# Kernel optimization log

Measured on AMD Instinct MI355X. Metric: run time of the kernel, lower is better.

The kernel has to match this reference:

```python
import jax, jax.numpy as jnp
import numpy as np

NUM_HEADS = 16
HIDDEN = 1024
HEAD = HIDDEN // NUM_HEADS


def setup_inputs() -> dict:
    key = jax.random.key(0)
    k1, k2, k3, k4, k5 = jax.random.split(key, 5)
    b, s, d = 2, 2048, HIDDEN
    scale = 1.0 / np.sqrt(d)
    return {
        "features": jax.random.normal(k1, (b, s, d), dtype=jnp.float32),
        "qkv_w": jax.random.normal(k2, (3 * d, d), dtype=jnp.float32) * scale,  # torch Linear weight [out,in]
        "qkv_b": jax.random.normal(k3, (3 * d,), dtype=jnp.float32) * 0.01,
        "out_w": jax.random.normal(k4, (d, d), dtype=jnp.float32) * scale,
        "out_b": jax.random.normal(k5, (d,), dtype=jnp.float32) * 0.01,
        "use_causal_mask": 0,
    }


def reference(features, qkv_w, qkv_b, out_w, out_b, use_causal_mask):
    b, s, d = features.shape
    qkv = features @ qkv_w.T + qkv_b                      # [b,s,3d]
    q, k, v = jnp.split(qkv, 3, axis=-1)
    # [b,s,d] -> [b,h,s,hd]
    def heads(x):
        return x.reshape(b, s, NUM_HEADS, HEAD).transpose(0, 2, 1, 3)
    q, k, v = heads(q), heads(k), heads(v)
    scores = jnp.einsum("bhqd,bhkd->bhqk", q, k) / np.sqrt(HEAD)
    if use_causal_mask:
        mask = jnp.triu(jnp.ones((s, s), dtype=bool), k=1)
        scores = jnp.where(mask, -jnp.inf, scores)
    attn = jax.nn.softmax(scores, axis=-1)
    out = jnp.einsum("bhqk,bhkd->bhqd", attn, v)          # [b,h,s,hd]
    out = out.transpose(0, 2, 1, 3).reshape(b, s, d)
    return out @ out_w.T + out_b
```

## Files before the change

### kernel.cpp

```cpp
#include <hip/hip_runtime.h>
#include <math.h>

#define BATCH 2
#define SEQ   2048
#define HID   1024
#define NHEAD 16
#define ROWS  (BATCH*SEQ)
#define QKV_N (3*HID)

#define Q_SCALE 0.18033688011112042f

typedef __attribute__((ext_vector_type(8))) short bf16x8;
typedef __attribute__((ext_vector_type(4))) float f32x4;

__device__ __forceinline__ unsigned short f2b(float f) {
    unsigned u = __float_as_uint(f);
    u += 0x7FFF + ((u >> 16) & 1);
    return (unsigned short)(u >> 16);
}
__device__ __forceinline__ unsigned pk2(float a, float b) {
    return (unsigned)f2b(a) | ((unsigned)f2b(b) << 16);
}

#define GLOAD_LDS16(gp, lp) \
    __builtin_amdgcn_global_load_lds((const __attribute__((address_space(1))) void*)(gp), \
                                     (__attribute__((address_space(3))) void*)(lp), 16, 0, 0)

__global__ __launch_bounds__(256)
void cvt_all(const float* __restrict__ a, unsigned short* __restrict__ oa, int na4,
             const float* __restrict__ b, unsigned short* __restrict__ ob, int nb4,
             const float* __restrict__ c, unsigned short* __restrict__ oc, int nc4) {
    int i = blockIdx.x * 256 + threadIdx.x;
    const float* src; unsigned short* dst; int j;
    if (i < na4)            { src = a; dst = oa; j = i; }
    else if (i < na4 + nb4) { src = b; dst = ob; j = i - na4; }
    else if (i < na4 + nb4 + nc4) { src = c; dst = oc; j = i - na4 - nb4; }
    else return;
    float4 v = reinterpret_cast<const float4*>(src)[j];
    ushort4 o;
    o.x = f2b(v.x); o.y = f2b(v.y); o.z = f2b(v.z); o.w = f2b(v.w);
    reinterpret_cast<ushort4*>(dst)[j] = o;
}

template<int MODE>
__global__ __launch_bounds__(256)
void gemm_mfma(const unsigned short* __restrict__ A, const unsigned short* __restrict__ B,
               const float* __restrict__ bias, void* __restrict__ Cout,
               unsigned short* __restrict__ vt, int M, int N, int K) {
    __shared__ __align__(16) unsigned short As[128 * 32];
    __shared__ __align__(16) unsigned short Bs[128 * 32];
    const int tid = threadIdx.x;
    const int w = tid >> 6, l = tid & 63;
    const int wm = w >> 1, wn = w & 1;
    const int l15 = l & 15, l4 = l >> 4;
    const long row0 = (long)blockIdx.y * 128;
    const long col0 = (long)blockIdx.x * 128;

    f32x4 acc[4][4];
    #pragma unroll
    for (int m = 0; m < 4; ++m)
        #pragma unroll
        for (int n = 0; n < 4; ++n) acc[m][n] = (f32x4)0.0f;

    const int lr   = l >> 2;
    const int slot = (l & 3) ^ (lr & 3);

    for (int k0 = 0; k0 < K; k0 += 32) {
        __syncthreads();
        #pragma unroll
        for (int c = 0; c < 2; ++c) {
            int r = w * 32 + c * 16 + lr;
            GLOAD_LDS16(A + (row0 + r) * K + k0 + slot * 8, As + (w * 32 + c * 16) * 32);
            GLOAD_LDS16(B + (col0 + r) * K + k0 + slot * 8, Bs + (w * 32 + c * 16) * 32);
        }
        __syncthreads();

        bf16x8 af[4], bfr[4];
        #pragma unroll
        for (int m = 0; m < 4; ++m) {
            int row = wm * 64 + m * 16 + l15;
            af[m] = *(const bf16x8*)((const char*)As + row * 64 + ((l4 ^ (row & 3)) << 4));
        }
        #pragma unroll
        for (int n = 0; n < 4; ++n) {
            int row = wn * 64 + n * 16 + l15;
            bfr[n] = *(const bf16x8*)((const char*)Bs + row * 64 + ((l4 ^ (row & 3)) << 4));
        }
        #pragma unroll
        for (int m = 0; m < 4; ++m)
            #pragma unroll
            for (int n = 0; n < 4; ++n)
                acc[m][n] = __builtin_amdgcn_mfma_f32_16x16x32_bf16(af[m], bfr[n], acc[m][n], 0, 0, 0);
    }

    #pragma unroll
    for (int m = 0; m < 4; ++m) {
        #pragma unroll
        for (int n = 0; n < 4; ++n) {
            long ccol = col0 + wn * 64 + n * 16 + l15;
            float bv = bias[ccol];
            #pragma unroll
            for (int r2 = 0; r2 < 4; ++r2) {
                long crow = row0 + wm * 64 + m * 16 + l4 * 4 + r2;
                float v = acc[m][n][r2] + bv;
                if (MODE == 0) {
                    ((float*)Cout)[crow * N + ccol] = v;
                } else {
                    if (ccol < 1024) {
                        ((unsigned short*)Cout)[crow * QKV_N + ccol] = f2b(v * Q_SCALE);
                    } else if (ccol < 2048) {
                        ((unsigned short*)Cout)[crow * QKV_N + ccol] = f2b(v);
                    } else {
                        long cc = ccol - 2048;
                        long h = cc >> 6, d = cc & 63;
                        long b = crow >> 11, s = crow & 2047;
                        vt[(((b * NHEAD + h) * 64 + d) << 11) + s] = f2b(v);
                    }
                }
            }
        }
    }
}

__global__ __launch_bounds__(256)
void attn_mfma(const unsigned short* __restrict__ qkv, const unsigned short* __restrict__ vt,
               unsigned short* __restrict__ attno, const int* __restrict__ use_mask) {
    __shared__ __align__(16) unsigned short Ks [64 * 64];
    __shared__ __align__(16) unsigned short Vts[64 * 64];
    __shared__ __align__(16) unsigned short Ps [4][16 * 64];
    const int tid = threadIdx.x;
    const int w = tid >> 6, l = tid & 63;
    const int l15 = l & 15, l4 = l >> 4;
    const int bid  = blockIdx.x;
    const int orig = (bid & 7) * 128 + (bid >> 3);
    const int qt = orig & 31, bh = orig >> 5;
    const int b = bh >> 4, h = bh & 15;
    const int q0 = qt * 64;
    const int wq0 = q0 + w * 16;
    const int causal = use_mask[0];
    const int NT = causal ? (qt + 1) : (SEQ / 64);

    bf16x8 qf[2];
    {
        const unsigned short* qp = qkv + (size_t)(b * SEQ + wq0 + l15) * QKV_N + h * 64;
        qf[0] = *(const bf16x8*)(qp + l4 * 8);
        qf[1] = *(const bf16x8*)(qp + 32 + l4 * 8);
    }

    f32x4 o_acc[4];
    #pragma unroll
    for (int n = 0; n < 4; ++n) o_acc[n] = (f32x4)0.0f;
    f32x4 l_acc = (f32x4)0.0f;

    bf16x8 ones;
    #pragma unroll
    for (int j = 0; j < 8; ++j) ones[j] = (short)0x3F80;

    const int srow = l >> 3, g = l & 7;
    const int r0   = w * 16 + srow;
    const int wso  = (g ^ srow) << 3;
    unsigned short* pw = Ps[w];

    const unsigned short* kp = qkv + (size_t)b * SEQ * QKV_N + HID + h * 64
                                   + (size_t)r0 * QKV_N + g * 8;
    const unsigned short* vp = vt + (size_t)bh * 64 * SEQ + (size_t)r0 * SEQ + g * 8;

    bf16x8 kreg[2], vreg[2];
    kreg[0] = *(const bf16x8*)(kp);
    kreg[1] = *(const bf16x8*)(kp + 8 * QKV_N);
    vreg[0] = *(const bf16x8*)(vp);
    vreg[1] = *(const bf16x8*)(vp + 8 * SEQ);
    kp += (size_t)64 * QKV_N;
    vp += 64;

    for (int kt = 0; kt < NT; ++kt) {
        __syncthreads();
        #pragma unroll
        for (int c = 0; c < 2; ++c) {
            *(bf16x8*)(Ks  + (r0 + c * 8) * 64 + wso) = kreg[c];
            *(bf16x8*)(Vts + (r0 + c * 8) * 64 + wso) = vreg[c];
        }
        __syncthreads();

        if (kt + 1 < NT) {
            kreg[0] = *(const bf16x8*)(kp);
            kreg[1] = *(const bf16x8*)(kp + 8 * QKV_N);
            vreg[0] = *(const bf16x8*)(vp);
            vreg[1] = *(const bf16x8*)(vp + 8 * SEQ);
            kp += (size_t)64 * QKV_N;
            vp += 64;
        }

        f32x4 s_acc[4];
        #pragma unroll
        for (int n = 0; n < 4; ++n) s_acc[n] = (f32x4)0.0f;
        __builtin_amdgcn_s_setprio(1);
        #pragma unroll
        for (int ks = 0; ks < 2; ++ks) {
            #pragma unroll
            for (int n = 0; n < 4; ++n) {
                int row = n * 16 + l15;
                bf16x8 kf = *(const bf16x8*)((const char*)Ks + row * 128 + (((ks * 4 + l4) ^ (row & 7)) << 4));
                s_acc[n] = __builtin_amdgcn_mfma_f32_16x16x32_bf16(kf, qf[ks], s_acc[n], 0, 0, 0);
            }
        }
        __builtin_amdgcn_s_setprio(0);
        if (causal) {
            int kk0 = kt * 64;
            #pragma unroll
            for (int n = 0; n < 4; ++n)
                #pragma unroll
                for (int r2 = 0; r2 < 4; ++r2) {
                    int krow = kk0 + n * 16 + l4 * 4 + r2;
                    int qcol = wq0 + l15;
                    if (krow > qcol) s_acc[n][r2] = -INFINITY;
                }
        }

        #pragma unroll
        for (int n = 0; n < 4; ++n) {
            float p0 = exp2f(s_acc[n][0]);
            float p1 = exp2f(s_acc[n][1]);
            float p2 = exp2f(s_acc[n][2]);
            float p3 = exp2f(s_acc[n][3]);
            uint2 pk;
            pk.x = pk2(p0, p1);
            pk.y = pk2(p2, p3);
            int byteoff = (n * 32 + l4 * 8) ^ ((l15 & 7) << 4);
            *(uint2*)((char*)pw + l15 * 128 + byteoff) = pk;
        }

        __builtin_amdgcn_s_setprio(1);
        #pragma unroll
        for (int ks = 0; ks < 2; ++ks) {
            bf16x8 pf = *(const bf16x8*)((const char*)pw + l15 * 128 + (((ks * 4 + l4) ^ (l15 & 7)) << 4));
            l_acc = __builtin_amdgcn_mfma_f32_16x16x32_bf16(pf, ones, l_acc, 0, 0, 0);
            #pragma unroll
            for (int n = 0; n < 4; ++n) {
                int vrow = n * 16 + l15;
                bf16x8 vf = *(const bf16x8*)((const char*)Vts + vrow * 128 + (((ks * 4 + l4) ^ (vrow & 7)) << 4));
                o_acc[n] = __builtin_amdgcn_mfma_f32_16x16x32_bf16(pf, vf, o_acc[n], 0, 0, 0);
            }
        }
        __builtin_amdgcn_s_setprio(0);
    }

    #pragma unroll
    for (int r2 = 0; r2 < 4; ++r2) {
        float inv = 1.0f / l_acc[r2];
        size_t orow = (size_t)(b * SEQ + wq0 + l4 * 4 + r2);
        #pragma unroll
        for (int n = 0; n < 4; ++n)
            attno[orow * HID + h * 64 + n * 16 + l15] = f2b(o_acc[n][r2] * inv);
    }
}

extern "C" void kernel_launch(void* const* d_in, const int* in_sizes, int n_in,
                              void* d_out, int out_size, void* d_ws, size_t ws_size,
                              hipStream_t stream) {
    const float* features = (const float*)d_in[0];
    const float* qkv_w    = (const float*)d_in[1];
    const float* qkv_b    = (const float*)d_in[2];
    const float* out_w    = (const float*)d_in[3];
    const float* out_b    = (const float*)d_in[4];
    const int*   use_mask = (const int*)d_in[5];

    char* ws = (char*)d_ws;
    unsigned short* fbf     = (unsigned short*)(ws);
    unsigned short* wbf     = (unsigned short*)(ws + 8388608);
    unsigned short* owbf    = (unsigned short*)(ws + 14680064);
    unsigned short* qkvbf   = (unsigned short*)(ws + 16777216);
    unsigned short* vtbuf   = (unsigned short*)(ws + 41943040);
    unsigned short* attnobf = (unsigned short*)(ws + 50331648);

    cvt_all<<<8192, 256, 0, stream>>>(features, fbf, 1048576,
                                      qkv_w, wbf, 786432,
                                      out_w, owbf, 262144);

    dim3 g1(QKV_N / 128, ROWS / 128);
    gemm_mfma<2><<<g1, 256, 0, stream>>>(fbf, wbf, qkv_b, (void*)qkvbf, vtbuf,
                                         ROWS, QKV_N, HID);

    attn_mfma<<<1024, 256, 0, stream>>>(qkvbf, vtbuf, attnobf, use_mask);

    dim3 g3(HID / 128, ROWS / 128);
    gemm_mfma<0><<<g3, 256, 0, stream>>>(attnobf, owbf, out_b, d_out, (unsigned short*)nullptr,
                                         ROWS, HID, HID);
}
```

Before: 157.9 us.

## Load K/V MFMA fragments directly from global memory, dropping LDS staging

Removes the shared-memory staging of K and V tiles and the two block-wide barriers per iteration. Each wave now loads its MFMA fragments straight from global memory, relying on L2/L1 because the four waves of a block share the same K/V tile. Launch bounds now request 4 blocks per SM to raise occupancy. The cost is four times as much redundant global/L1 traffic, and the register-prefetch double buffering is gone, so load latency is exposed each iteration unless occupancy hides it.

Result: slower. 306.8 us (+94.3%).

```diff
diff --git a/kernel.cpp b/kernel.cpp
--- a/kernel.cpp
+++ b/kernel.cpp
@@ -122,12 +122,10 @@
     }
 }
 
-__global__ __launch_bounds__(256)
+__global__ __launch_bounds__(256, 4)
 void attn_mfma(const unsigned short* __restrict__ qkv, const unsigned short* __restrict__ vt,
                unsigned short* __restrict__ attno, const int* __restrict__ use_mask) {
-    __shared__ __align__(16) unsigned short Ks [64 * 64];
-    __shared__ __align__(16) unsigned short Vts[64 * 64];
-    __shared__ __align__(16) unsigned short Ps [4][16 * 64];
+    __shared__ __align__(16) unsigned short Ps[4][16 * 64];
     const int tid = threadIdx.x;
     const int w = tid >> 6, l = tid & 63;
     const int l15 = l & 15, l4 = l >> 4;
@@ -156,55 +154,38 @@
     #pragma unroll
     for (int j = 0; j < 8; ++j) ones[j] = (short)0x3F80;
 
-    const int srow = l >> 3, g = l & 7;
-    const int r0   = w * 16 + srow;
-    const int wso  = (g ^ srow) << 3;
     unsigned short* pw = Ps[w];
 
-    const unsigned short* kp = qkv + (size_t)b * SEQ * QKV_N + HID + h * 64
-                                   + (size_t)r0 * QKV_N + g * 8;
-    const unsigned short* vp = vt + (size_t)bh * 64 * SEQ + (size_t)r0 * SEQ + g * 8;
-
-    bf16x8 kreg[2], vreg[2];
-    kreg[0] = *(const bf16x8*)(kp);
-    kreg[1] = *(const bf16x8*)(kp + 8 * QKV_N);
-    vreg[0] = *(const bf16x8*)(vp);
-    vreg[1] = *(const bf16x8*)(vp + 8 * SEQ);
-    kp += (size_t)64 * QKV_N;
-    vp += 64;
+    const unsigned short* kq = qkv + (size_t)b * SEQ * QKV_N + HID + h * 64
+                                   + (size_t)l15 * QKV_N + l4 * 8;
+    const unsigned short* vq = vt + (size_t)bh * 64 * SEQ + (size_t)l15 * SEQ + l4 * 8;
 
     for (int kt = 0; kt < NT; ++kt) {
-        __syncthreads();
-        #pragma unroll
-        for (int c = 0; c < 2; ++c) {
-            *(bf16x8*)(Ks  + (r0 + c * 8) * 64 + wso) = kreg[c];
-            *(bf16x8*)(Vts + (r0 + c * 8) * 64 + wso) = vreg[c];
-        }
-        __syncthreads();
-
-        if (kt + 1 < NT) {
-            kreg[0] = *(const bf16x8*)(kp);
-            kreg[1] = *(const bf16x8*)(kp + 8 * QKV_N);
-            vreg[0] = *(const bf16x8*)(vp);
-            vreg[1] = *(const bf16x8*)(vp + 8 * SEQ);
-            kp += (size_t)64 * QKV_N;
-            vp += 64;
-        }
+        bf16x8 kf[2][4];
+        #pragma unroll
+        for (int ks = 0; ks < 2; ++ks)
+            #pragma unroll
+            for (int n = 0; n < 4; ++n)
+                kf[ks][n] = *(const bf16x8*)(kq + (size_t)n * 16 * QKV_N + ks * 32);
 
         f32x4 s_acc[4];
         #pragma unroll
         for (int n = 0; n < 4; ++n) s_acc[n] = (f32x4)0.0f;
         __builtin_amdgcn_s_setprio(1);
         #pragma unroll
-        for (int ks = 0; ks < 2; ++ks) {
-            #pragma unroll
-            for (int n = 0; n < 4; ++n) {
-                int row = n * 16 + l15;
-                bf16x8 kf = *(const bf16x8*)((const char*)Ks + row * 128 + (((ks * 4 + l4) ^ (row & 7)) << 4));
-                s_acc[n] = __builtin_amdgcn_mfma_f32_16x16x32_bf16(kf, qf[ks], s_acc[n], 0, 0, 0);
-            }
-        }
+        for (int ks = 0; ks < 2; ++ks)
+            #pragma unroll
+            for (int n = 0; n < 4; ++n)
+                s_acc[n] = __builtin_amdgcn_mfma_f32_16x16x32_bf16(kf[ks][n], qf[ks], s_acc[n], 0, 0, 0);
         __builtin_amdgcn_s_setprio(0);
+
+        bf16x8 vf[2][4];
+        #pragma unroll
+        for (int ks = 0; ks < 2; ++ks)
+            #pragma unroll
+            for (int n = 0; n < 4; ++n)
+                vf[ks][n] = *(const bf16x8*)(vq + (size_t)n * 16 * SEQ + ks * 32);
+
         if (causal) {
             int kk0 = kt * 64;
             #pragma unroll
@@ -236,13 +217,13 @@
             bf16x8 pf = *(const bf16x8*)((const char*)pw + l15 * 128 + (((ks * 4 + l4) ^ (l15 & 7)) << 4));
             l_acc = __builtin_amdgcn_mfma_f32_16x16x32_bf16(pf, ones, l_acc, 0, 0, 0);
             #pragma unroll
-            for (int n = 0; n < 4; ++n) {
-                int vrow = n * 16 + l15;
-                bf16x8 vf = *(const bf16x8*)((const char*)Vts + vrow * 128 + (((ks * 4 + l4) ^ (vrow & 7)) << 4));
-                o_acc[n] = __builtin_amdgcn_mfma_f32_16x16x32_bf16(pf, vf, o_acc[n], 0, 0, 0);
-            }
+            for (int n = 0; n < 4; ++n)
+                o_acc[n] = __builtin_amdgcn_mfma_f32_16x16x32_bf16(pf, vf[ks][n], o_acc[n], 0, 0, 0);
         }
         __builtin_amdgcn_s_setprio(0);
+
+        kq += (size_t)64 * QKV_N;
+        vq += 64;
     }
 
     #pragma unroll
```
